# Optimization experiments

Measured on AMD Instinct MI355X. Metric: run time of the kernel, lower is better.

The kernel has to match this reference:

```python
import jax, jax.numpy as jnp
import numpy as np

N = 10000          # num_stations / nodes
E = 320000         # edges
IN_DIM = 32
HID = 64
SEQ = 168
OUT_DIM = 10000


def _gcn_conv(x, W, b, src, dst, num_nodes):
    """PyG GCNConv: add self-loops, sym-normalize, gather-scatter aggregate."""
    loop = jnp.arange(num_nodes)
    s = jnp.concatenate([src, loop])
    d = jnp.concatenate([dst, loop])
    deg = jax.ops.segment_sum(jnp.ones_like(d, dtype=x.dtype), d, num_segments=num_nodes)
    dinv = jnp.where(deg > 0, jax.lax.rsqrt(deg), 0.0)
    norm = dinv[s] * dinv[d]                      # [E+N]
    h = x @ W.T                                   # [N, out] linear (no bias inside)
    msg = h[s] * norm[:, None]                    # gather + scale
    out = jax.ops.segment_sum(msg, d, num_segments=num_nodes)  # scatter-add
    return out + b


def setup_inputs() -> dict:
    key = jax.random.key(0)
    ks = jax.random.split(key, 16)
    sc = 0.05
    return {
        "x": jax.random.normal(ks[0], (N, IN_DIM), jnp.float32),
        "edge_index": jax.random.randint(ks[1], (2, E), 0, N, jnp.int64),
        "rain_history": jax.random.normal(ks[2], (1, SEQ), jnp.float32),
        "future_rain": jax.random.normal(ks[3], (1, 1), jnp.float32),
        "W1": jax.random.normal(ks[4], (HID, IN_DIM), jnp.float32) * sc,
        "b1": jnp.zeros((HID,), jnp.float32),
        "W2": jax.random.normal(ks[5], (HID, HID), jnp.float32) * sc,
        "b2": jnp.zeros((HID,), jnp.float32),
        "wf1_W": jax.random.normal(ks[6], (HID, SEQ + 1), jnp.float32) * sc,
        "wf1_b": jnp.zeros((HID,), jnp.float32),
        "wf2_W": jax.random.normal(ks[7], (HID, HID), jnp.float32) * sc,
        "wf2_b": jnp.zeros((HID,), jnp.float32),
        "of1_W": jax.random.normal(ks[8], (HID * 2, HID * N + HID), jnp.float32) * 0.001,
        "of1_b": jnp.zeros((HID * 2,), jnp.float32),
        "of2_W": jax.random.normal(ks[9], (OUT_DIM, HID * 2), jnp.float32) * sc,
        "of2_b": jnp.zeros((OUT_DIM,), jnp.float32),
    }


def reference(x, edge_index, rain_history, future_rain,
              W1, b1, W2, b2, wf1_W, wf1_b, wf2_W, wf2_b,
              of1_W, of1_b, of2_W, of2_b):
    src, dst = edge_index[0], edge_index[1]
    num_nodes = x.shape[0]
    h = jax.nn.relu(_gcn_conv(x, W1, b1, src, dst, num_nodes))
    h = jax.nn.relu(_gcn_conv(h, W2, b2, src, dst, num_nodes))
    h = jnp.clip(h, -10.0, 10.0)
    node_features = h.reshape(1, -1)                        # [1, N*HID]
    weather_input = jnp.concatenate([rain_history, future_rain], axis=1)  # [1, SEQ+1]
    w = jax.nn.relu(weather_input @ wf1_W.T + wf1_b)
    weather_features = w @ wf2_W.T + wf2_b                  # [1, HID]
    combined = jnp.concatenate([node_features, weather_features], axis=1)
    o = jax.nn.relu(combined @ of1_W.T + of1_b)
    out = o @ of2_W.T + of2_b                               # [1, OUT_DIM]
    return out.squeeze(0)
```

## Files before the change

### kernel.cpp

```cpp
#include <hip/hip_runtime.h>
#include <hip/hip_bf16.h>

#define N_NODES 10000
#define N_EDGES 320000
#define HID 64
#define IN_DIM 32
#define SEQ 168
#define OUT_DIM 10000
#define OF1_COLS 640064
#define NODE_COLS 640000
#define NODE_NV   160000
#define OF1_SPLITS 64
#define OF1_CHUNK  2500
#define OF1_ROWS   8
#define BUCKET 128

typedef __attribute__((ext_vector_type(4))) float f32x4;

__global__ __launch_bounds__(256) void k_fill_weather(
        const int* __restrict__ eidx, int* __restrict__ cursor, int* __restrict__ csr,
        const float* __restrict__ rain, const float* __restrict__ fut,
        const float* __restrict__ w1W, const float* __restrict__ w1b,
        const float* __restrict__ w2W, const float* __restrict__ w2b,
        const float* __restrict__ of1W, float* __restrict__ wtail) {
    int t = threadIdx.x;
    if (blockIdx.x < (N_EDGES + 255) / 256) {
        int e = blockIdx.x * 256 + t;
        if (e < N_EDGES) {
            int s = eidx[e];
            int d = eidx[N_EDGES + e];
            int slot = atomicAdd(&cursor[d], 1);
            csr[d * BUCKET + slot] = s;
        }
    } else {
        __shared__ float wi[SEQ + 1];
        __shared__ float w1[64];
        __shared__ float wf[64];
        if (t < SEQ) wi[t] = rain[t];
        if (t == SEQ) wi[SEQ] = fut[0];
        __syncthreads();
        if (t < 64) {
            float acc = w1b[t];
            for (int i = 0; i < SEQ + 1; i++) acc += w1W[t * (SEQ + 1) + i] * wi[i];
            w1[t] = fmaxf(acc, 0.f);
        }
        __syncthreads();
        if (t < 64) {
            float acc2 = w2b[t];
#pragma unroll
            for (int i = 0; i < 64; i++) acc2 += w2W[t * 64 + i] * w1[i];
            wf[t] = acc2;
        }
        __syncthreads();
        if (t < 128) {
            const float* Wt = of1W + (size_t)t * OF1_COLS + NODE_COLS;
            float s = 0.f;
#pragma unroll
            for (int w = 0; w < 64; w++) s += Wt[w] * wf[w];
            wtail[t] = s;
        }
    }
}

__global__ __launch_bounds__(256) void k_lin1(const float* __restrict__ x, const float* __restrict__ W,
                                              const int* __restrict__ cnt, float* __restrict__ hlin) {
    __shared__ float Wl[64][33];
    __shared__ float xs[4][32];
    int t = threadIdx.x;
    for (int i = t; i < 64 * 32; i += 256) Wl[i >> 5][i & 31] = W[i];
    int node0 = blockIdx.x * 4;
    if (t < 128) {
        int n = t >> 5, k = t & 31;
        xs[n][k] = x[(node0 + n) * IN_DIM + k];
    }
    __syncthreads();
    int nl = t >> 6, j = t & 63;
    float acc = 0.f;
#pragma unroll
    for (int k = 0; k < 32; k++) acc += xs[nl][k] * Wl[j][k];
    float dn = rsqrtf((float)(cnt[node0 + nl] + 1));
    hlin[(node0 + nl) * HID + j] = acc * dn;
}

__global__ __launch_bounds__(256) void k_lin2(const float* __restrict__ h1, const float* __restrict__ W,
                                              const int* __restrict__ cnt, float* __restrict__ hlin) {
    __shared__ float Wl[64][65];
    __shared__ float xs[4][64];
    int t = threadIdx.x;
    for (int i = t; i < 64 * 64; i += 256) Wl[i >> 6][i & 63] = W[i];
    int node0 = blockIdx.x * 4;
    int nl = t >> 6, j = t & 63;
    xs[nl][j] = h1[(node0 + nl) * HID + j];
    __syncthreads();
    float acc = 0.f;
#pragma unroll
    for (int k = 0; k < 64; k++) acc += xs[nl][k] * Wl[j][k];
    float dn = rsqrtf((float)(cnt[node0 + nl] + 1));
    hlin[(node0 + nl) * HID + j] = acc * dn;
}

__global__ __launch_bounds__(256) void k_agg(const float* __restrict__ hlin, const int* __restrict__ cnt,
                                             const int* __restrict__ csr,
                                             const float* __restrict__ bias, float* __restrict__ out, int doClip) {
    int wave = (blockIdx.x * 256 + threadIdx.x) >> 6;
    int lane = threadIdx.x & 63;
    if (wave >= N_NODES) return;
    int deg = cnt[wave];
    float acc = hlin[wave * HID + lane];
    const int* row = csr + wave * BUCKET;
    for (int base = 0; base < deg; base += 64) {
        int idx = base + lane;
        int sv = row[(idx < deg) ? idx : 0];
        int m = deg - base;
        if (m > 64) m = 64;
        for (int j = 0; j < m; j++) {
            int s = __shfl(sv, j, 64);
            acc += hlin[s * HID + lane];
        }
    }
    float dn = rsqrtf((float)(deg + 1));
    float v = dn * acc + bias[lane];
    v = fmaxf(v, 0.f);
    if (doClip) v = fminf(v, 10.f);
    out[wave * HID + lane] = v;
}

__global__ __launch_bounds__(256) void k_of1(const float* __restrict__ W, const float* __restrict__ comb,
                                             float* __restrict__ o_pre) {
    int split = blockIdx.x;
    int j0 = blockIdx.y * OF1_ROWS;
    int i0 = split * OF1_CHUNK;
    int i1 = i0 + OF1_CHUNK;
    const f32x4* C4 = (const f32x4*)comb;
    const f32x4* Wr[OF1_ROWS];
#pragma unroll
    for (int r = 0; r < OF1_ROWS; r++)
        Wr[r] = (const f32x4*)(W + (size_t)(j0 + r) * OF1_COLS);
    float a[OF1_ROWS];
#pragma unroll
    for (int r = 0; r < OF1_ROWS; r++) a[r] = 0.f;
    for (int i = i0 + threadIdx.x; i < i1; i += 256) {
        f32x4 cv = C4[i];
#pragma unroll
        for (int r = 0; r < OF1_ROWS; r++) {
            f32x4 wv = __builtin_nontemporal_load(&Wr[r][i]);
            a[r] += wv.x * cv.x + wv.y * cv.y + wv.z * cv.z + wv.w * cv.w;
        }
    }
#pragma unroll
    for (int off = 1; off < 64; off <<= 1) {
#pragma unroll
        for (int r = 0; r < OF1_ROWS; r++) a[r] += __shfl_xor(a[r], off, 64);
    }
    __shared__ float red[4][OF1_ROWS];
    int lane = threadIdx.x & 63, wid = threadIdx.x >> 6;
    if (lane == 0) {
#pragma unroll
        for (int r = 0; r < OF1_ROWS; r++) red[wid][r] = a[r];
    }
    __syncthreads();
    if (threadIdx.x < OF1_ROWS)
        atomicAdd(&o_pre[j0 + threadIdx.x],
                  red[0][threadIdx.x] + red[1][threadIdx.x] + red[2][threadIdx.x] + red[3][threadIdx.x]);
}

__global__ __launch_bounds__(256) void k_of2(const float* __restrict__ W, const float* __restrict__ of2b,
                                             const float* __restrict__ o_pre, const float* __restrict__ of1b,
                                             const float* __restrict__ wtail, float* __restrict__ out) {
    __shared__ float os[128];
    int t = threadIdx.x;
    if (t < 128) os[t] = fmaxf(o_pre[t] + of1b[t] + wtail[t], 0.f);
    __syncthreads();
    int k = blockIdx.x * 256 + t;
    if (k >= OUT_DIM) return;
    const f32x4* Wr = (const f32x4*)(W + (size_t)k * 128);
    float acc = of2b[k];
#pragma unroll
    for (int i = 0; i < 32; i++) {
        f32x4 wv = __builtin_nontemporal_load(&Wr[i]);
        int base = i * 4;
        acc += wv.x * os[base + 0] + wv.y * os[base + 1] + wv.z * os[base + 2] + wv.w * os[base + 3];
    }
    out[k] = acc;
}

extern "C" void kernel_launch(void* const* d_in, const int* in_sizes, int n_in,
                              void* d_out, int out_size, void* d_ws, size_t ws_size,
                              hipStream_t stream) {
    const float* x    = (const float*)d_in[0];
    const int*  eidx  = (const int*)d_in[1];
    const float* rain = (const float*)d_in[2];
    const float* fut  = (const float*)d_in[3];
    const float* W1   = (const float*)d_in[4];
    const float* b1   = (const float*)d_in[5];
    const float* W2   = (const float*)d_in[6];
    const float* b2   = (const float*)d_in[7];
    const float* wf1W = (const float*)d_in[8];
    const float* wf1b = (const float*)d_in[9];
    const float* wf2W = (const float*)d_in[10];
    const float* wf2b = (const float*)d_in[11];
    const float* of1W = (const float*)d_in[12];
    const float* of1b = (const float*)d_in[13];
    const float* of2W = (const float*)d_in[14];
    const float* of2b = (const float*)d_in[15];
    float* out = (float*)d_out;

    char* p = (char*)d_ws;
    int*   cursor = (int*)(p + 0);
    float* o_pre  = (float*)(p + 40000);
    int*   csr    = (int*)(p + 40960);
    float* hlin   = (float*)(p + 5242880);
    float* h1     = (float*)(p + 7864320);
    float* comb   = (float*)(p + 10485760);
    float* wtail  = (float*)(p + 13107200);

    hipMemsetAsync(p, 0, 40512, stream);

    k_fill_weather<<<(N_EDGES + 255) / 256 + 1, 256, 0, stream>>>(
        eidx, cursor, csr, rain, fut, wf1W, wf1b, wf2W, wf2b, of1W, wtail);

    k_lin1<<<N_NODES / 4, 256, 0, stream>>>(x, W1, cursor, hlin);
    k_agg<<<N_NODES / 4, 256, 0, stream>>>(hlin, cursor, csr, b1, h1, 0);
    k_lin2<<<N_NODES / 4, 256, 0, stream>>>(h1, W2, cursor, hlin);
    k_agg<<<N_NODES / 4, 256, 0, stream>>>(hlin, cursor, csr, b2, comb, 1);

    k_of1<<<dim3(OF1_SPLITS, 128 / OF1_ROWS), 256, 0, stream>>>(of1W, comb, o_pre);
    k_of2<<<(OUT_DIM + 255) / 256, 256, 0, stream>>>(of2W, of2b, o_pre, of1b, wtail, out);
}
```

Baseline: 545.4 us.

## Fuse GCN layers into fewer kernels with per-source normalization in aggregation

Merges the first linear layer into the CSR-fill/weather kernel by moving the source-degree normalization out of the linear step and into aggregation, where each lane computes a per-neighbor rsqrt and shuffles it across the wave. It also fuses layer-1 aggregation with the layer-2 linear transform through shared memory, and unrolls the neighbor gather loop by four. This cuts kernel launches and one intermediate global round trip. In exchange, aggregation does an extra gather of neighbor degree counts.

```diff
diff --git a/kernel.cpp b/kernel.cpp
--- a/kernel.cpp
+++ b/kernel.cpp
@@ -1,5 +1,4 @@
 #include <hip/hip_runtime.h>
-#include <hip/hip_bf16.h>
 
 #define N_NODES 10000
 #define N_EDGES 320000
@@ -14,24 +13,43 @@
 #define OF1_CHUNK  2500
 #define OF1_ROWS   8
 #define BUCKET 128
+#define FILLB  1250
+#define LIN1B  2500
 
 typedef __attribute__((ext_vector_type(4))) float f32x4;
 
-__global__ __launch_bounds__(256) void k_fill_weather(
+__global__ __launch_bounds__(256) void k_fill_lin1_weather(
         const int* __restrict__ eidx, int* __restrict__ cursor, int* __restrict__ csr,
+        const float* __restrict__ x, const float* __restrict__ W1, float* __restrict__ hlin,
         const float* __restrict__ rain, const float* __restrict__ fut,
         const float* __restrict__ w1W, const float* __restrict__ w1b,
         const float* __restrict__ w2W, const float* __restrict__ w2b,
         const float* __restrict__ of1W, float* __restrict__ wtail) {
     int t = threadIdx.x;
-    if (blockIdx.x < (N_EDGES + 255) / 256) {
-        int e = blockIdx.x * 256 + t;
+    int b = blockIdx.x;
+    if (b < FILLB) {
+        int e = b * 256 + t;
         if (e < N_EDGES) {
             int s = eidx[e];
             int d = eidx[N_EDGES + e];
             int slot = atomicAdd(&cursor[d], 1);
             csr[d * BUCKET + slot] = s;
         }
+    } else if (b < FILLB + LIN1B) {
+        __shared__ float Wl[64][33];
+        __shared__ float xs[4][32];
+        for (int i = t; i < 64 * 32; i += 256) Wl[i >> 5][i & 31] = W1[i];
+        int node0 = (b - FILLB) * 4;
+        if (t < 128) {
+            int n = t >> 5, k = t & 31;
+            xs[n][k] = x[(node0 + n) * IN_DIM + k];
+        }
+        __syncthreads();
+        int nl = t >> 6, j = t & 63;
+        float acc = 0.f;
+#pragma unroll
+        for (int k = 0; k < 32; k++) acc += xs[nl][k] * Wl[j][k];
+        hlin[(node0 + nl) * HID + j] = acc;
     } else {
         __shared__ float wi[SEQ + 1];
         __shared__ float w1[64];
@@ -62,67 +80,88 @@
     }
 }
 
-__global__ __launch_bounds__(256) void k_lin1(const float* __restrict__ x, const float* __restrict__ W,
-                                              const int* __restrict__ cnt, float* __restrict__ hlin) {
-    __shared__ float Wl[64][33];
-    __shared__ float xs[4][32];
-    int t = threadIdx.x;
-    for (int i = t; i < 64 * 32; i += 256) Wl[i >> 5][i & 31] = W[i];
-    int node0 = blockIdx.x * 4;
-    if (t < 128) {
-        int n = t >> 5, k = t & 31;
-        xs[n][k] = x[(node0 + n) * IN_DIM + k];
-    }
-    __syncthreads();
-    int nl = t >> 6, j = t & 63;
-    float acc = 0.f;
-#pragma unroll
-    for (int k = 0; k < 32; k++) acc += xs[nl][k] * Wl[j][k];
-    float dn = rsqrtf((float)(cnt[node0 + nl] + 1));
-    hlin[(node0 + nl) * HID + j] = acc * dn;
-}
-
-__global__ __launch_bounds__(256) void k_lin2(const float* __restrict__ h1, const float* __restrict__ W,
-                                              const int* __restrict__ cnt, float* __restrict__ hlin) {
+__global__ __launch_bounds__(256) void k_agg1_lin2(
+        const float* __restrict__ hlin, const int* __restrict__ cnt,
+        const int* __restrict__ csr, const float* __restrict__ b1,
+        const float* __restrict__ W2, float* __restrict__ h2) {
     __shared__ float Wl[64][65];
     __shared__ float xs[4][64];
     int t = threadIdx.x;
-    for (int i = t; i < 64 * 64; i += 256) Wl[i >> 6][i & 63] = W[i];
-    int node0 = blockIdx.x * 4;
-    int nl = t >> 6, j = t & 63;
-    xs[nl][j] = h1[(node0 + nl) * HID + j];
-    __syncthreads();
-    float acc = 0.f;
-#pragma unroll
-    for (int k = 0; k < 64; k++) acc += xs[nl][k] * Wl[j][k];
-    float dn = rsqrtf((float)(cnt[node0 + nl] + 1));
-    hlin[(node0 + nl) * HID + j] = acc * dn;
-}
-
-__global__ __launch_bounds__(256) void k_agg(const float* __restrict__ hlin, const int* __restrict__ cnt,
-                                             const int* __restrict__ csr,
-                                             const float* __restrict__ bias, float* __restrict__ out, int doClip) {
-    int wave = (blockIdx.x * 256 + threadIdx.x) >> 6;
-    int lane = threadIdx.x & 63;
-    if (wave >= N_NODES) return;
-    int deg = cnt[wave];
-    float acc = hlin[wave * HID + lane];
-    const int* row = csr + wave * BUCKET;
+    for (int i = t; i < 64 * 64; i += 256) Wl[i >> 6][i & 63] = W2[i];
+    int wid = t >> 6, lane = t & 63;
+    int n = blockIdx.x * 4 + wid;
+    int deg = cnt[n];
+    float dn = rsqrtf((float)(deg + 1));
+    float acc = hlin[n * HID + lane] * dn;
+    const int* row = csr + n * BUCKET;
     for (int base = 0; base < deg; base += 64) {
         int idx = base + lane;
         int sv = row[(idx < deg) ? idx : 0];
+        float dv = (idx < deg) ? rsqrtf((float)(cnt[sv] + 1)) : 0.f;
         int m = deg - base;
         if (m > 64) m = 64;
-        for (int j = 0; j < m; j++) {
-            int s = __shfl(sv, j, 64);
-            acc += hlin[s * HID + lane];
-        }
-    }
+        int m4 = (m + 3) & ~3;
+        for (int j = 0; j < m4; j += 4) {
+            int s0 = __shfl(sv, j, 64), s1 = __shfl(sv, j + 1, 64);
+            int s2 = __shfl(sv, j + 2, 64), s3 = __shfl(sv, j + 3, 64);
+            float d0 = __shfl(dv, j, 64), d1 = __shfl(dv, j + 1, 64);
+            float d2 = __shfl(dv, j + 2, 64), d3 = __shfl(dv, j + 3, 64);
+            float v0 = hlin[s0 * HID + lane];
+            float v1 = hlin[s1 * HID + lane];
+            float v2 = hlin[s2 * HID + lane];
+            float v3 = hlin[s3 * HID + lane];
+            acc = fmaf(d0, v0, acc);
+            acc = fmaf(d1, v1, acc);
+            acc = fmaf(d2, v2, acc);
+            acc = fmaf(d3, v3, acc);
+        }
+    }
+    float v = fmaxf(dn * acc + b1[lane], 0.f);
+    xs[wid][lane] = v;
+    __syncthreads();
+    float a2 = 0.f;
+#pragma unroll
+    for (int k = 0; k < 64; k++) a2 += xs[wid][k] * Wl[lane][k];
+    h2[n * HID + lane] = a2;
+}
+
+__global__ __launch_bounds__(256) void k_agg2(
+        const float* __restrict__ h2, const int* __restrict__ cnt,
+        const int* __restrict__ csr, const float* __restrict__ b2,
+        float* __restrict__ comb) {
+    int t = threadIdx.x;
+    int wid = t >> 6, lane = t & 63;
+    int n = blockIdx.x * 4 + wid;
+    int deg = cnt[n];
     float dn = rsqrtf((float)(deg + 1));
-    float v = dn * acc + bias[lane];
+    float acc = h2[n * HID + lane] * dn;
+    const int* row = csr + n * BUCKET;
+    for (int base = 0; base < deg; base += 64) {
+        int idx = base + lane;
+        int sv = row[(idx < deg) ? idx : 0];
+        float dv = (idx < deg) ? rsqrtf((float)(cnt[sv] + 1)) : 0.f;
+        int m = deg - base;
+        if (m > 64) m = 64;
+        int m4 = (m + 3) & ~3;
+        for (int j = 0; j < m4; j += 4) {
+            int s0 = __shfl(sv, j, 64), s1 = __shfl(sv, j + 1, 64);
+            int s2 = __shfl(sv, j + 2, 64), s3 = __shfl(sv, j + 3, 64);
+            float d0 = __shfl(dv, j, 64), d1 = __shfl(dv, j + 1, 64);
+            float d2 = __shfl(dv, j + 2, 64), d3 = __shfl(dv, j + 3, 64);
+            float v0 = h2[s0 * HID + lane];
+            float v1 = h2[s1 * HID + lane];
+            float v2 = h2[s2 * HID + lane];
+            float v3 = h2[s3 * HID + lane];
+            acc = fmaf(d0, v0, acc);
+            acc = fmaf(d1, v1, acc);
+            acc = fmaf(d2, v2, acc);
+            acc = fmaf(d3, v3, acc);
+        }
+    }
+    float v = dn * acc + b2[lane];
     v = fmaxf(v, 0.f);
-    if (doClip) v = fminf(v, 10.f);
-    out[wave * HID + lane] = v;
+    v = fminf(v, 10.f);
+    comb[n * HID + lane] = v;
 }
 
 __global__ __launch_bounds__(256) void k_of1(const float* __restrict__ W, const float* __restrict__ comb,
@@ -210,19 +249,17 @@
     float* o_pre  = (float*)(p + 40000);
     int*   csr    = (int*)(p + 40960);
     float* hlin   = (float*)(p + 5242880);
-    float* h1     = (float*)(p + 7864320);
+    float* h2     = (float*)(p + 7864320);
     float* comb   = (float*)(p + 10485760);
     float* wtail  = (float*)(p + 13107200);
 
     hipMemsetAsync(p, 0, 40512, stream);
 
-    k_fill_weather<<<(N_EDGES + 255) / 256 + 1, 256, 0, stream>>>(
-        eidx, cursor, csr, rain, fut, wf1W, wf1b, wf2W, wf2b, of1W, wtail);
-
-    k_lin1<<<N_NODES / 4, 256, 0, stream>>>(x, W1, cursor, hlin);
-    k_agg<<<N_NODES / 4, 256, 0, stream>>>(hlin, cursor, csr, b1, h1, 0);
-    k_lin2<<<N_NODES / 4, 256, 0, stream>>>(h1, W2, cursor, hlin);
-    k_agg<<<N_NODES / 4, 256, 0, stream>>>(hlin, cursor, csr, b2, comb, 1);
+    k_fill_lin1_weather<<<FILLB + LIN1B + 1, 256, 0, stream>>>(
+        eidx, cursor, csr, x, W1, hlin, rain, fut, wf1W, wf1b, wf2W, wf2b, of1W, wtail);
+
+    k_agg1_lin2<<<N_NODES / 4, 256, 0, stream>>>(hlin, cursor, csr, b1, W2, h2);
+    k_agg2<<<N_NODES / 4, 256, 0, stream>>>(h2, cursor, csr, b2, comb);
 
     k_of1<<<dim3(OF1_SPLITS, 128 / OF1_ROWS), 256, 0, stream>>>(of1W, comb, o_pre);
     k_of2<<<(OUT_DIM + 255) / 256, 256, 0, stream>>>(of2W, of2b, o_pre, of1b, wtail, out);
```

New measurement: 520.9 us. 1.05x faster.
